# Kernel tuning notes

Hardware: AMD Instinct MI355X
Metric: run time of the kernel (lower is better)

The kernel has to match this reference:

```python
import jax, jax.numpy as jnp
import numpy as np

B, NUM_CLASSES, H, W, CF = 2, 19, 64, 64, 256
TOPK_IDX = 20  # hard-coded in the torch source: sorted descending value at index 20


def _cosine(x):
    # x: [B, N, D] -> clamped cosine affinity [B, N, N]
    xn = x / (jnp.linalg.norm(x, axis=2, keepdims=True) + 1e-9)
    return jnp.maximum(jnp.einsum('bnd,bmd->bnm', xn, xn), 0.0)


def _conv1x1(x, w, b):
    # x: [B, C, H, W], w: [O, C], b: [O]
    return jnp.einsum('bchw,oc->bohw', x, w) + b[None, :, None, None]


def setup_inputs() -> dict:
    key = jax.random.key(0)
    ks = jax.random.split(key, 12)
    s_c = (2.0 / NUM_CLASSES) ** 0.5  # kaiming fan_in scale for 1x1 conv
    s_f = (2.0 / CF) ** 0.5
    return {
        'pred': jax.random.normal(ks[0], (B, NUM_CLASSES, H, W), jnp.float32),
        'feat': jax.random.normal(ks[1], (B, CF, H, W), jnp.float32),
        'w_cls1': jax.random.normal(ks[2], (NUM_CLASSES, NUM_CLASSES), jnp.float32) * s_c,
        'b_cls1': jnp.zeros((NUM_CLASSES,), jnp.float32),
        'w_cls2': jax.random.normal(ks[3], (NUM_CLASSES, NUM_CLASSES), jnp.float32) * s_c,
        'b_cls2': jnp.zeros((NUM_CLASSES,), jnp.float32),
        'w_pro1': jax.random.normal(ks[4], (CF, CF), jnp.float32) * s_f,
        'b_pro1': jnp.zeros((CF,), jnp.float32),
        'w_pro2': jax.random.normal(ks[5], (CF, CF), jnp.float32) * s_f,
        'b_pro2': jnp.zeros((CF,), jnp.float32),
        'class_weight': jnp.ones((NUM_CLASSES,), jnp.float32),
    }


def reference(pred, feat, w_cls1, b_cls1, w_cls2, b_cls2,
              w_pro1, b_pro1, w_pro2, b_pro2, class_weight):
    bsz, c, h, w = feat.shape
    C = pred.shape[1]
    N = h * w
    feat_flat = feat.reshape(bsz, c, N).transpose(0, 2, 1)  # [B, N, 256]

    # --- no_grad block 1: confidence mask + top-k sparsified cosine affinity ---
    prob = jax.nn.softmax(pred, axis=1)
    p_prob = prob.max(axis=1)      # [B, H, W]
    p_max = prob.argmax(axis=1)    # [B, H, W]
    cwm = class_weight / (class_weight.max() + 1e-10) * 0.95
    mask = ((p_prob >= 0.95) | (p_prob >= cwm[p_max])).astype(jnp.float32)
    mask = jax.lax.stop_gradient(mask.reshape(bsz, N, 1))  # broadcast over classes

    aff1 = _cosine(feat_flat)                                # [B, N, N]
    thr = -jnp.sort(-aff1, axis=-1)[:, :, TOPK_IDX:TOPK_IDX + 1]  # per-row 21st largest
    aff1 = jnp.where(aff1 < thr, 0.0, aff1)
    aff1 = jax.lax.stop_gradient(aff1 + aff1.transpose(0, 2, 1))

    # --- degree-normalized propagation of predictions ---
    pred_flat = pred.reshape(bsz, C, N).transpose(0, 2, 1)   # [B, N, C]
    d1 = (aff1.sum(-1) + 1e-10) ** -0.5                      # D^{-1/2}
    aff1n = d1[:, :, None] * aff1 * d1[:, None, :]           # D^{-1/2} A D^{-1/2}
    p2 = jnp.einsum('bnm,bmc->bnc', aff1n, pred_flat)
    p3 = (0.8 * p2 + 0.2 * pred_flat) * (1.0 - mask) + (0.2 * p2 + 0.8 * pred_flat) * mask
    pred2 = p3.transpose(0, 2, 1).reshape(bsz, C, h, w)
    pred_out = _conv1x1(_conv1x1(pred2, w_cls1, b_cls1), w_cls2, b_cls2)

    # --- no_grad block 2: class-consistency-masked affinity over refined softmax ---
    oh = jax.nn.one_hot(p_max, C, dtype=jnp.float32)         # [B, H, W, C]
    # faithful to torch: permute(0,2,3,1) on the already-[B,H,W,C] one-hot, then flat view
    oh = jnp.transpose(oh, (0, 2, 3, 1)).reshape(bsz, -1, C)
    sp = jax.nn.softmax(pred_out, axis=1).reshape(bsz, C, N).transpose(0, 2, 1)
    aff_f = _cosine(sp)
    aff_f = jnp.where(_cosine(oh) == 0.0, 0.0, aff_f)
    d2 = (aff_f.sum(-1) + 1e-10) ** -0.5
    aff_fn = jax.lax.stop_gradient(d2[:, :, None] * aff_f * d2[:, None, :])

    # --- propagate features and project ---
    new_feat = jnp.einsum('bnm,bmc->bnc', aff_fn, feat_flat)
    new_feat = new_feat.transpose(0, 2, 1).reshape(bsz, c, h, w)
    feat_out = _conv1x1(jax.nn.relu(_conv1x1(new_feat, w_pro1, b_pro1)), w_pro2, b_pro2)
    return pred_out, feat_out
```

## Files before the change

kernel.cpp:

```cpp
#include <hip/hip_runtime.h>

#define NN 4096
#define DD 256
#define CC 19
#define BB 2

typedef __attribute__((ext_vector_type(8))) short bf16x8;
typedef _Float16 f16x8 __attribute__((ext_vector_type(8)));
typedef __attribute__((ext_vector_type(4))) float f32x4;

#define GLL16(gp, lp) __builtin_amdgcn_global_load_lds( \
    (const __attribute__((address_space(1))) unsigned int*)(gp), \
    (__attribute__((address_space(3))) unsigned int*)(lp), 16, 0, 0)

__device__ inline unsigned short f2b(float f) {
  unsigned int u = __float_as_uint(f);
  return (unsigned short)((u + 0x7FFFu + ((u >> 16) & 1u)) >> 16);
}
__device__ inline float b2f(unsigned short h) {
  return __uint_as_float(((unsigned int)h) << 16);
}
__device__ inline unsigned int pack2(float a, float b) {
  return (unsigned int)f2b(a) | ((unsigned int)f2b(b) << 16);
}
__device__ inline void split16(float x, unsigned short& h, unsigned short& l) {
  _Float16 hh = (_Float16)x;
  float hf = (float)hh;
  _Float16 ll = (_Float16)((x - hf) * 2048.0f);
  h = *reinterpret_cast<unsigned short*>(&hh);
  l = *reinterpret_cast<unsigned short*>(&ll);
}

__global__ __launch_bounds__(256) void k_prep(const float* __restrict__ pred,
                                              const float* __restrict__ cw,
                                              const float* __restrict__ feat,
                                              float* __restrict__ maskb,
                                              unsigned int* __restrict__ ohbits,
                                              unsigned short* __restrict__ xh,
                                              unsigned short* __restrict__ xl) {
  int g = blockIdx.x * 256 + threadIdx.x;
  int b = g >> 12, n = g & (NN - 1);
  {
    const float* p = pred + (size_t)b * CC * NN + n;
    float v[CC];
    float mx = -1e30f; int am = 0;
#pragma unroll
    for (int c = 0; c < CC; ++c) {
      float t = p[(size_t)c * NN];
      v[c] = t;
      if (t > mx) { mx = t; am = c; }
    }
    float s = 0.f;
#pragma unroll
    for (int c = 0; c < CC; ++c) s += expf(v[c] - mx);
    float pprob = 1.f / s;
    float cmax = 0.f;
#pragma unroll
    for (int c = 0; c < CC; ++c) cmax = fmaxf(cmax, cw[c]);
    float cwm = cw[am] / (cmax + 1e-10f) * 0.95f;
    maskb[g] = (pprob >= 0.95f || pprob >= cwm) ? 1.f : 0.f;
    int h = n >> 6, w = n & 63;
    int L = w * (CC * 64) + am * 64 + h;
    atomicOr(&ohbits[b * NN + L / CC], 1u << (L % CC));
  }
  {
    const float* f = feat + (size_t)b * DD * NN + n;
    float s = 0.f;
    for (int d = 0; d < DD; ++d) { float t = f[(size_t)d * NN]; s += t * t; }
    float r = 1.f / (sqrtf(s) + 1e-9f);
    size_t ob = ((size_t)b * NN + n) * DD;
    for (int d = 0; d < DD; d += 4) {
      ushort4 oh, ol;
      split16(f[(size_t)d * NN] * r, oh.x, ol.x);
      split16(f[(size_t)(d + 1) * NN] * r, oh.y, ol.y);
      split16(f[(size_t)(d + 2) * NN] * r, oh.z, ol.z);
      split16(f[(size_t)(d + 3) * NN] * r, oh.w, ol.w);
      *reinterpret_cast<ushort4*>(&xh[ob + d]) = oh;
      *reinterpret_cast<ushort4*>(&xl[ob + d]) = ol;
    }
  }
}

__global__ __launch_bounds__(256, 2) void k_gram1(const unsigned short* __restrict__ xh,
                                                  const unsigned short* __restrict__ xl,
                                                  float* __restrict__ M) {
  int Lh = blockIdx.x;
  int L = (Lh & 7) * 66 + (Lh >> 3);
  int b = blockIdx.y;
  int I = 0;
  while (L >= 32 - I) { L -= 32 - I; ++I; }
  int J = I + L;
  int i0 = I * 128, j0 = J * 128;
  float* Mb = M + (size_t)b * NN * NN;
  const unsigned short* XH = xh + (size_t)b * NN * DD;
  const unsigned short* XL = xl + (size_t)b * NN * DD;
  __shared__ unsigned short stage[2][4][128][32];
  int t = threadIdx.x;
  int wave = t >> 6, lane = t & 63;
  int wr = (wave & 1) * 64, wc = (wave >> 1) * 64;
  int lrow = lane & 15, quad = lane >> 4;
  int sel = (lrow >> 1) & 3;
  f32x4 accH[4][4] = {}, accL[4][4] = {};
  const unsigned short* src = (wave == 0) ? XH + (size_t)i0 * DD
                             : (wave == 1) ? XL + (size_t)i0 * DD
                             : (wave == 2) ? XH + (size_t)j0 * DD
                                           : XL + (size_t)j0 * DD;
  int srow = lane >> 2;
  int spart = (lane & 3) ^ ((lane >> 3) & 3);
#pragma unroll
  for (int e = 0; e < 8; ++e)
    GLL16(&src[(size_t)(e * 16 + srow) * DD + spart * 8], &stage[0][wave][e * 16][0]);
  __syncthreads();
  int cur = 0;
  for (int k0 = 0; k0 < DD; k0 += 32) {
    if (k0 + 32 < DD) {
#pragma unroll
      for (int e = 0; e < 8; ++e)
        GLL16(&src[(size_t)(e * 16 + srow) * DD + k0 + 32 + spart * 8],
              &stage[cur ^ 1][wave][e * 16][0]);
    }
    f16x8 ah[4], al[4], bh[4], bl[4];
#pragma unroll
    for (int i = 0; i < 4; ++i) {
      int ra = wr + i * 16 + lrow;
      int rb = wc + i * 16 + lrow;
      int sl = (quad ^ sel) * 8;
      ah[i] = *reinterpret_cast<const f16x8*>(&stage[cur][0][ra][sl]);
      al[i] = *reinterpret_cast<const f16x8*>(&stage[cur][1][ra][sl]);
      bh[i] = *reinterpret_cast<const f16x8*>(&stage[cur][2][rb][sl]);
      bl[i] = *reinterpret_cast<const f16x8*>(&stage[cur][3][rb][sl]);
    }
#pragma unroll
    for (int i = 0; i < 4; ++i) {
#pragma unroll
      for (int j = 0; j < 4; ++j) {
        accH[i][j] = __builtin_amdgcn_mfma_f32_16x16x32_f16(ah[i], bh[j], accH[i][j], 0, 0, 0);
        accL[i][j] = __builtin_amdgcn_mfma_f32_16x16x32_f16(ah[i], bl[j], accL[i][j], 0, 0, 0);
        accL[i][j] = __builtin_amdgcn_mfma_f32_16x16x32_f16(al[i], bh[j], accL[i][j], 0, 0, 0);
      }
    }
    __syncthreads();
    cur ^= 1;
  }
#pragma unroll
  for (int i = 0; i < 4; ++i)
#pragma unroll
    for (int j = 0; j < 4; ++j)
#pragma unroll
      for (int reg = 0; reg < 4; ++reg)
        accH[i][j][reg] = fmaxf(accH[i][j][reg] + accL[i][j][reg] * 4.8828125e-4f, 0.f);
  float* buf = (float*)stage;
  int rr = t >> 4, cc = t & 15;
  for (int half = 0; half < 2; ++half) {
    __syncthreads();
    if ((wr >> 6) == half) {
#pragma unroll
      for (int i = 0; i < 4; ++i)
#pragma unroll
        for (int j = 0; j < 4; ++j)
#pragma unroll
          for (int reg = 0; reg < 4; ++reg)
            buf[(i * 16 + quad * 4 + reg) * 132 + wc + j * 16 + lrow] = accH[i][j][reg];
    }
    __syncthreads();
#pragma unroll
    for (int i = 0; i < 4; ++i) {
      int row = rr + i * 16;
#pragma unroll
      for (int q = 0; q < 2; ++q) {
        int col = cc * 4 + q * 64;
        *reinterpret_cast<float4*>(&Mb[(size_t)(i0 + half * 64 + row) * NN + j0 + col]) =
            *reinterpret_cast<float4*>(&buf[row * 132 + col]);
      }
    }
  }
  if (I != J) {
    for (int half = 0; half < 2; ++half) {
      __syncthreads();
      if ((wc >> 6) == half) {
#pragma unroll
        for (int i = 0; i < 4; ++i)
#pragma unroll
          for (int j = 0; j < 4; ++j)
#pragma unroll
            for (int reg = 0; reg < 4; ++reg)
              buf[(j * 16 + lrow) * 132 + wr + i * 16 + quad * 4 + reg] = accH[i][j][reg];
      }
      __syncthreads();
#pragma unroll
      for (int i = 0; i < 4; ++i) {
        int row = rr + i * 16;
#pragma unroll
        for (int q = 0; q < 2; ++q) {
          int col = cc * 4 + q * 64;
          *reinterpret_cast<float4*>(&Mb[(size_t)(j0 + half * 64 + row) * NN + i0 + col]) =
              *reinterpret_cast<float4*>(&buf[row * 132 + col]);
        }
      }
    }
  }
}

__global__ __launch_bounds__(256, 2) void k_topk(const float* __restrict__ M,
                                                 float* __restrict__ thr) {
  __shared__ unsigned int cbuf[4][64];
  int b = blockIdx.y;
  int wave = threadIdx.x >> 6, lane = threadIdx.x & 63;
  int n = blockIdx.x * 4 + wave;
  const float* row = M + (size_t)b * NN * NN + (size_t)n * NN;
  uint4 v[16];
#pragma unroll
  for (int e = 0; e < 16; ++e) {
    unsigned long long addr = (unsigned long long)(row + lane * 4 + e * 256);
    asm volatile("global_load_dwordx4 %0, %1, off" : "=v"(v[e]) : "v"(addr));
  }
  asm volatile("s_waitcnt vmcnt(0)" ::: "memory");
  __builtin_amdgcn_sched_barrier(0);
  unsigned int mx = 0u;
#pragma unroll
  for (int e = 0; e < 16; ++e) {
    unsigned int a = v[e].x > v[e].y ? v[e].x : v[e].y;
    unsigned int c2 = v[e].z > v[e].w ? v[e].z : v[e].w;
    a = a > c2 ? a : c2;
    mx = mx > a ? mx : a;
  }
  unsigned int lo = 0u, hi = 0x3FC00000u;
  while (lo < hi) {
    unsigned int mid = lo + ((hi - lo + 1) >> 1);
    if (__popcll(__ballot(mx >= mid)) >= 21) lo = mid; else hi = mid - 1;
  }
  unsigned int s = lo;
  unsigned int base = 0;
  unsigned long long ltmask = (1ull << lane) - 1ull;
#pragma unroll
  for (int e = 0; e < 16; ++e) {
#pragma unroll
    for (int q = 0; q < 4; ++q) {
      unsigned int val = (q == 0) ? v[e].x : (q == 1) ? v[e].y : (q == 2) ? v[e].z : v[e].w;
      unsigned long long mk = __ballot(val >= s);
      if (mk) {
        unsigned int pos = base + (unsigned int)__popcll(mk & ltmask);
        if (val >= s && pos < 64u) cbuf[wave][pos] = val;
        base += (unsigned int)__popcll(mk);
      }
    }
  }
  asm volatile("s_waitcnt lgkmcnt(0)" ::: "memory");
  __builtin_amdgcn_sched_barrier(0);
  unsigned int t = s;
  if (base <= 64u) {
    unsigned int cand = (lane < (int)base) ? cbuf[wave][lane] : 0u;
    lo = s; hi = 0x3FC00000u;
    while (lo < hi) {
      unsigned int mid = lo + ((hi - lo + 1) >> 1);
      if (__popcll(__ballot(cand >= mid)) >= 21) lo = mid; else hi = mid - 1;
    }
    t = lo;
  }
  {
    unsigned int t1 = t + 1u;
    int c1 = 0, c2 = 0;
#pragma unroll
    for (int e = 0; e < 16; ++e) {
      c1 += (int)__popcll(__ballot(v[e].x >= t));
      c1 += (int)__popcll(__ballot(v[e].y >= t));
      c1 += (int)__popcll(__ballot(v[e].z >= t));
      c1 += (int)__popcll(__ballot(v[e].w >= t));
      c2 += (int)__popcll(__ballot(v[e].x >= t1));
      c2 += (int)__popcll(__ballot(v[e].y >= t1));
      c2 += (int)__popcll(__ballot(v[e].z >= t1));
      c2 += (int)__popcll(__ballot(v[e].w >= t1));
    }
    if (!(c1 >= 21 && c2 < 21)) {
      lo = 0u; hi = 0x40000000u;
      while (lo < hi) {
        unsigned int mid = lo + ((hi - lo + 1) >> 1);
        int c = 0;
#pragma unroll
        for (int e = 0; e < 16; ++e) {
          c += (int)__popcll(__ballot(v[e].x >= mid));
          c += (int)__popcll(__ballot(v[e].y >= mid));
          c += (int)__popcll(__ballot(v[e].z >= mid));
          c += (int)__popcll(__ballot(v[e].w >= mid));
        }
        if (c >= 21) lo = mid; else hi = mid - 1;
      }
      t = lo;
    }
  }
  if (lane == 0) thr[b * NN + n] = __uint_as_float(t);
}

__global__ __launch_bounds__(256) void k_symm(float* __restrict__ M, const float* __restrict__ thr,
                                              float* __restrict__ dsum) {
  int L = blockIdx.x;
  int b = blockIdx.y;
  int I = 0;
  while (L >= 64 - I) { L -= 64 - I; ++I; }
  int J = I + L;
  float* Mb = M + (size_t)b * NN * NN;
  unsigned short* Mus = (unsigned short*)Mb;
  const float* th = thr + b * NN;
  __shared__ float A[64][65];
  int t = threadIdx.x;
  int i0 = I * 64, j0 = J * 64;
  float areg[16];
#pragma unroll
  for (int e = 0; e < 16; ++e) {
    int lin = t + e * 256;
    int i = lin >> 6, j = lin & 63;
    areg[e] = Mb[(size_t)(i0 + i) * NN + j0 + j];
  }
#pragma unroll
  for (int e = 0; e < 16; ++e) {
    int lin = t + e * 256;
    int i = lin >> 6, j = lin & 63;
    float a = areg[e];
    float v = a * ((a >= th[i0 + i] ? 1.f : 0.f) + (a >= th[j0 + j] ? 1.f : 0.f));
    A[i][j] = v;
  }
  __syncthreads();
  {
    int i = t >> 2, seg = (t & 3) * 16;
    float v[16];
#pragma unroll
    for (int q = 0; q < 4; ++q)
      *reinterpret_cast<float4*>(&v[q * 4]) = *reinterpret_cast<float4*>(&A[i][seg + q * 4]);
    unsigned int pk[8];
#pragma unroll
    for (int q = 0; q < 8; ++q) pk[q] = pack2(v[2 * q], v[2 * q + 1]);
    size_t ub = 2 * (size_t)(i0 + i) * NN + 2 * (size_t)j0 + seg;
    *reinterpret_cast<int4*>(&Mus[ub])     = *reinterpret_cast<int4*>(&pk[0]);
    *reinterpret_cast<int4*>(&Mus[ub + 8]) = *reinterpret_cast<int4*>(&pk[4]);
  }
  if (I != J) {
    int j = t >> 2, seg = (t & 3) * 16;
    float v[16];
#pragma unroll
    for (int e = 0; e < 16; ++e) v[e] = A[seg + e][j];
    unsigned int pk[8];
#pragma unroll
    for (int q = 0; q < 8; ++q) pk[q] = pack2(v[2 * q], v[2 * q + 1]);
    size_t ub = 2 * (size_t)(j0 + j) * NN + 2 * (size_t)i0 + seg;
    *reinterpret_cast<int4*>(&Mus[ub])     = *reinterpret_cast<int4*>(&pk[0]);
    *reinterpret_cast<int4*>(&Mus[ub + 8]) = *reinterpret_cast<int4*>(&pk[4]);
  }
  if (t < 64) {
    float s = 0.f;
#pragma unroll
    for (int j = 0; j < 64; ++j) s += A[t][j];
    atomicAdd(&dsum[b * NN + i0 + t], s);
  } else if (t < 128 && I != J) {
    int j = t - 64;
    float s = 0.f;
#pragma unroll
    for (int i = 0; i < 64; ++i) s += A[i][j];
    atomicAdd(&dsum[b * NN + j0 + j], s);
  }
}

__global__ void k_make_yb(const float* __restrict__ pred, const float* __restrict__ d1,
                          unsigned short* __restrict__ ybh) {
  int g = blockIdx.x * 256 + threadIdx.x;
  int idx = g * 4;
  int b = idx / (32 * NN);
  int c = (idx / NN) & 31;
  int n = idx & (NN - 1);
  ushort4 o = make_ushort4(0, 0, 0, 0);
  if (c < CC) {
    float4 p = *reinterpret_cast<const float4*>(&pred[((size_t)b * CC + c) * NN + n]);
    const float* dd = d1 + b * NN + n;
    o.x = f2b(p.x * (1.f / sqrtf(dd[0] + 1e-10f)));
    o.y = f2b(p.y * (1.f / sqrtf(dd[1] + 1e-10f)));
    o.z = f2b(p.z * (1.f / sqrtf(dd[2] + 1e-10f)));
    o.w = f2b(p.w * (1.f / sqrtf(dd[3] + 1e-10f)));
  }
  *reinterpret_cast<ushort4*>(&ybh[idx]) = o;
}

__global__ __launch_bounds__(256, 2) void k_p2_mfma(
    const float* __restrict__ M, const unsigned short* __restrict__ ybh,
    const float* __restrict__ d1, float* __restrict__ p2b) {
  int b = blockIdx.y;
  int n0 = blockIdx.x * 64;
  const unsigned short* Mus = (const unsigned short*)(M + (size_t)b * NN * NN);
  const unsigned short* Y = ybh + (size_t)b * 32 * NN;
  __shared__ unsigned short As2[2][64][64];
  __shared__ unsigned short Ys2[2][32][64];
  int t = threadIdx.x;
  int wave = t >> 6, lane = t & 63;
  int wn = (wave & 1) * 32;
  int wc = (wave >> 1) * 16;
  int lrow = lane & 15, quad = lane >> 4;
  f32x4 acc[2] = {{0.f,0.f,0.f,0.f},{0.f,0.f,0.f,0.f}};
  int lr3 = lane >> 3;
  int srow = wave * 8 + lr3;
  int spart = (lane & 7) ^ lr3;
#pragma unroll
  for (int e = 0; e < 2; ++e)
    GLL16(&Mus[2 * (size_t)(n0 + e * 32 + srow) * NN + spart * 8],
          &As2[0][e * 32 + wave * 8][0]);
  GLL16(&Y[(size_t)srow * NN + spart * 8], &Ys2[0][wave * 8][0]);
  __syncthreads();
  int cur = 0;
  for (int m0 = 0; m0 < NN; m0 += 64) {
    if (m0 + 64 < NN) {
#pragma unroll
      for (int e = 0; e < 2; ++e)
        GLL16(&Mus[2 * (size_t)(n0 + e * 32 + srow) * NN + 2 * (size_t)(m0 + 64) + spart * 8],
              &As2[cur ^ 1][e * 32 + wave * 8][0]);
      GLL16(&Y[(size_t)srow * NN + m0 + 64 + spart * 8], &Ys2[cur ^ 1][wave * 8][0]);
    }
#pragma unroll
    for (int kc = 0; kc < 2; ++kc) {
      int sl = ((kc * 4 + quad) ^ (lrow & 7)) * 8;
      bf16x8 bfr = *reinterpret_cast<const bf16x8*>(&Ys2[cur][wc + lrow][sl]);
#pragma unroll
      for (int i = 0; i < 2; ++i) {
        bf16x8 af = *reinterpret_cast<const bf16x8*>(&As2[cur][wn + i * 16 + lrow][sl]);
        acc[i] = __builtin_amdgcn_mfma_f32_16x16x32_bf16(af, bfr, acc[i], 0, 0, 0);
      }
    }
    __syncthreads();
    cur ^= 1;
  }
  int c = wc + lrow;
  if (c < CC) {
#pragma unroll
    for (int i = 0; i < 2; ++i) {
#pragma unroll
      for (int reg = 0; reg < 4; ++reg) {
        int n = n0 + wn + i * 16 + quad * 4 + reg;
        float dv = 1.f / sqrtf(d1[b * NN + n] + 1e-10f);
        p2b[((size_t)b * NN + n) * CC + c] = dv * acc[i][reg];
      }
    }
  }
}

__global__ __launch_bounds__(64) void k_pred_head(const float* __restrict__ pred,
    const float* __restrict__ p2b, const float* __restrict__ maskb,
    const float* __restrict__ w1, const float* __restrict__ b1,
    const float* __restrict__ w2, const float* __restrict__ b2,
    float* __restrict__ out, unsigned short* __restrict__ spnP) {
  __shared__ float sw1[CC * CC], sw2[CC * CC], sb1[CC], sb2[CC];
  int t = threadIdx.x;
  for (int i = t; i < CC * CC; i += 64) { sw1[i] = w1[i]; sw2[i] = w2[i]; }
  if (t < CC) { sb1[t] = b1[t]; sb2[t] = b2[t]; }
  __syncthreads();
  int g = blockIdx.x * 64 + t;
  int b = g >> 12, n = g & (NN - 1);
  float m = maskb[g];
  float ca = (m > 0.5f) ? 0.2f : 0.8f;
  float cb = (m > 0.5f) ? 0.8f : 0.2f;
  const float* P = pred + (size_t)b * CC * NN + n;
  const float* Q = p2b + (size_t)g * CC;
  float p3[CC];
#pragma unroll
  for (int c = 0; c < CC; ++c) p3[c] = ca * Q[c] + cb * P[(size_t)c * NN];
  float midv[CC];
#pragma unroll
  for (int o = 0; o < CC; ++o) {
    float s = sb1[o];
#pragma unroll
    for (int c = 0; c < CC; ++c) s += sw1[o * CC + c] * p3[c];
    midv[o] = s;
  }
  float ov[CC];
  float mx = -1e30f;
#pragma unroll
  for (int o = 0; o < CC; ++o) {
    float s = sb2[o];
#pragma unroll
    for (int c = 0; c < CC; ++c) s += sw2[o * CC + c] * midv[c];
    ov[o] = s;
    out[(size_t)b * CC * NN + (size_t)o * NN + n] = s;
    mx = fmaxf(mx, s);
  }
  float se = 0.f;
  float e[CC];
#pragma unroll
  for (int o = 0; o < CC; ++o) { e[o] = expf(ov[o] - mx); se += e[o]; }
  float inv = 1.f / se;
  float nrm = 0.f;
#pragma unroll
  for (int o = 0; o < CC; ++o) { float sp = e[o] * inv; e[o] = sp; nrm += sp * sp; }
  float rn = 1.f / (sqrtf(nrm) + 1e-9f);
  unsigned short sp[32];
#pragma unroll
  for (int o = 0; o < CC; ++o) sp[o] = f2b(e[o] * rn);
#pragma unroll
  for (int o = CC; o < 32; ++o) sp[o] = 0;
  unsigned short* dst = spnP + (size_t)g * 32;
#pragma unroll
  for (int q = 0; q < 4; ++q)
    *reinterpret_cast<int4*>(&dst[q * 8]) = *reinterpret_cast<int4*>(&sp[q * 8]);
}

__global__ __launch_bounds__(256) void k_gram2(const unsigned short* __restrict__ spnP,
    const unsigned int* __restrict__ bits, unsigned short* __restrict__ Mh,
    float* __restrict__ d2) {
  int L = blockIdx.x;
  int b = blockIdx.y;
  int I = 0;
  while (L >= 64 - I) { L -= 64 - I; ++I; }
  int J = I + L;
  const unsigned short* X = spnP + (size_t)b * NN * 32;
  unsigned short* Mb = Mh + (size_t)b * NN * NN;
  __shared__ unsigned short As[64][32], Bs[64][32];
  __shared__ unsigned short tr[64][66];
  __shared__ unsigned int bI[64], bJ[64];
  int t = threadIdx.x;
  int wave = t >> 6, lane = t & 63;
  int lrow = lane & 15, quad = lane >> 4;
  int i0 = I * 64, j0 = J * 64;
  int srow = wave * 16 + (lane >> 2);
  int spart = (lane & 3) ^ ((lane >> 3) & 3);
  GLL16(&X[(size_t)(i0 + srow) * 32 + spart * 8], &As[wave * 16][0]);
  GLL16(&X[(size_t)(j0 + srow) * 32 + spart * 8], &Bs[wave * 16][0]);
  if (t < 64) bI[t] = bits[b * NN + i0 + t];
  else if (t < 128) bJ[t - 64] = bits[b * NN + j0 + t - 64];
  __syncthreads();
  int wi = wave & 1, wj = wave >> 1;
  int sl = (quad ^ ((lrow >> 1) & 3)) * 8;
  bf16x8 af[2], bfr[2];
#pragma unroll
  for (int i = 0; i < 2; ++i) {
    af[i]  = *reinterpret_cast<const bf16x8*>(&As[wi * 32 + i * 16 + lrow][sl]);
    bfr[i] = *reinterpret_cast<const bf16x8*>(&Bs[wj * 32 + i * 16 + lrow][sl]);
  }
  f32x4 acc[2][2] = {{{0.f,0.f,0.f,0.f},{0.f,0.f,0.f,0.f}},{{0.f,0.f,0.f,0.f},{0.f,0.f,0.f,0.f}}};
#pragma unroll
  for (int i = 0; i < 2; ++i)
#pragma unroll
    for (int j = 0; j < 2; ++j)
      acc[i][j] = __builtin_amdgcn_mfma_f32_16x16x32_bf16(af[i], bfr[j], acc[i][j], 0, 0, 0);
#pragma unroll
  for (int i = 0; i < 2; ++i) {
#pragma unroll
    for (int j = 0; j < 2; ++j) {
#pragma unroll
      for (int reg = 0; reg < 4; ++reg) {
        int row = wi * 32 + i * 16 + quad * 4 + reg;
        int col = wj * 32 + j * 16 + lrow;
        bool keep = (bI[row] & bJ[col]) != 0u;
        float v = keep ? fmaxf(acc[i][j][reg], 0.f) : 0.f;
        tr[row][col] = f2b(v);
      }
    }
  }
  __syncthreads();
  {
    int row = t >> 2, seg = (t & 3) * 16;
    unsigned int w[8];
#pragma unroll
    for (int k = 0; k < 8; ++k)
      w[k] = *reinterpret_cast<const unsigned int*>(&tr[row][seg + 2 * k]);
    *reinterpret_cast<int4*>(&Mb[(size_t)(i0 + row) * NN + j0 + seg])     =
        *reinterpret_cast<int4*>(&w[0]);
    *reinterpret_cast<int4*>(&Mb[(size_t)(i0 + row) * NN + j0 + seg + 8]) =
        *reinterpret_cast<int4*>(&w[4]);
  }
  if (I != J) {
#pragma unroll
    for (int e = 0; e < 16; ++e) {
      int lin = t + e * 256;
      int jr = lin >> 6, ic = lin & 63;
      Mb[(size_t)(j0 + jr) * NN + i0 + ic] = tr[ic][jr];
    }
  }
  if (t < 64) {
    float s = 0.f;
#pragma unroll
    for (int c = 0; c < 64; ++c) s += b2f(tr[t][c]);
    atomicAdd(&d2[b * NN + i0 + t], s);
  } else if (t < 128 && I != J) {
    int c = t - 64;
    float s = 0.f;
#pragma unroll
    for (int i = 0; i < 64; ++i) s += b2f(tr[i][c]);
    atomicAdd(&d2[b * NN + j0 + c], s);
  }
}

__global__ void k_make_z(const float* __restrict__ feat, const float* __restrict__ d2,
                         unsigned short* __restrict__ zb,
                         const float* __restrict__ w1, const float* __restrict__ w2,
                         unsigned short* __restrict__ wb1, unsigned short* __restrict__ wb2) {
  int g = blockIdx.x * 256 + threadIdx.x;
  int idx = g * 4;
  int b = idx / (DD * NN);
  int m = idx & (NN - 1);
  float4 f = *reinterpret_cast<const float4*>(&feat[idx]);
  const float* dd = d2 + b * NN + m;
  ushort4 o;
  o.x = f2b(f.x * (1.f / sqrtf(dd[0] + 1e-10f)));
  o.y = f2b(f.y * (1.f / sqrtf(dd[1] + 1e-10f)));
  o.z = f2b(f.z * (1.f / sqrtf(dd[2] + 1e-10f)));
  o.w = f2b(f.w * (1.f / sqrtf(dd[3] + 1e-10f)));
  *reinterpret_cast<ushort4*>(&zb[idx]) = o;
  if (blockIdx.x < DD * DD / (4 * 256)) {
    int wi = idx;
    float4 a = *reinterpret_cast<const float4*>(&w1[wi]);
    float4 c = *reinterpret_cast<const float4*>(&w2[wi]);
    ushort4 oa, oc;
    oa.x = f2b(a.x); oa.y = f2b(a.y); oa.z = f2b(a.z); oa.w = f2b(a.w);
    oc.x = f2b(c.x); oc.y = f2b(c.y); oc.z = f2b(c.z); oc.w = f2b(c.w);
    *reinterpret_cast<ushort4*>(&wb1[wi]) = oa;
    *reinterpret_cast<ushort4*>(&wb2[wi]) = oc;
  }
}

__global__ __launch_bounds__(256, 2) void k_newfeat_mfma(
    const unsigned short* __restrict__ Mh, const unsigned short* __restrict__ zb,
    const float* __restrict__ d2, unsigned short* __restrict__ nfh) {
  int b = blockIdx.z;
  int nblk = blockIdx.x;
  int dblk = blockIdx.y;
  const unsigned short* A = zb + (size_t)b * DD * NN + (size_t)(dblk * 64) * NN;
  const unsigned short* Bm = Mh + (size_t)b * NN * NN + (size_t)(nblk * 64) * NN;
  __shared__ unsigned short As[2][64][64];
  __shared__ unsigned short Bs[2][64][64];
  int t = threadIdx.x;
  int wave = t >> 6, lane = t & 63;
  int wd = (wave & 1) * 32, wn = (wave >> 1) * 32;
  int lrow = lane & 15, quad = lane >> 4;
  f32x4 acc[2][2] = {{{0.f,0.f,0.f,0.f},{0.f,0.f,0.f,0.f}},{{0.f,0.f,0.f,0.f},{0.f,0.f,0.f,0.f}}};
  int lr3 = lane >> 3;
  int srow = wave * 8 + lr3;
  int spart = (lane & 7) ^ lr3;
#pragma unroll
  for (int e = 0; e < 2; ++e) {
    GLL16(&A [(size_t)(e * 32 + srow) * NN + spart * 8], &As[0][e * 32 + wave * 8][0]);
    GLL16(&Bm[(size_t)(e * 32 + srow) * NN + spart * 8], &Bs[0][e * 32 + wave * 8][0]);
  }
  __syncthreads();
  int cur = 0;
  for (int m0 = 0; m0 < NN; m0 += 64) {
    if (m0 + 64 < NN) {
#pragma unroll
      for (int e = 0; e < 2; ++e) {
        GLL16(&A [(size_t)(e * 32 + srow) * NN + m0 + 64 + spart * 8],
              &As[cur ^ 1][e * 32 + wave * 8][0]);
        GLL16(&Bm[(size_t)(e * 32 + srow) * NN + m0 + 64 + spart * 8],
              &Bs[cur ^ 1][e * 32 + wave * 8][0]);
      }
    }
#pragma unroll
    for (int kc = 0; kc < 2; ++kc) {
      int sl = ((kc * 4 + quad) ^ (lrow & 7)) * 8;
      bf16x8 af[2], bfr[2];
#pragma unroll
      for (int i = 0; i < 2; ++i) {
        af[i]  = *reinterpret_cast<const bf16x8*>(&As[cur][wd + i * 16 + lrow][sl]);
        bfr[i] = *reinterpret_cast<const bf16x8*>(&Bs[cur][wn + i * 16 + lrow][sl]);
      }
#pragma unroll
      for (int i = 0; i < 2; ++i)
#pragma unroll
        for (int j = 0; j < 2; ++j)
          acc[i][j] = __builtin_amdgcn_mfma_f32_16x16x32_bf16(af[i], bfr[j], acc[i][j], 0, 0, 0);
    }
    __syncthreads();
    cur ^= 1;
  }
#pragma unroll
  for (int j = 0; j < 2; ++j) {
    int n = nblk * 64 + wn + j * 16 + lrow;
    float sc = 1.f / sqrtf(d2[b * NN + n] + 1e-10f);
#pragma unroll
    for (int i = 0; i < 2; ++i) {
      int d = dblk * 64 + wd + i * 16 + quad * 4;
      ushort4 o;
      o.x = f2b(acc[i][j].x * sc); o.y = f2b(acc[i][j].y * sc);
      o.z = f2b(acc[i][j].z * sc); o.w = f2b(acc[i][j].w * sc);
      *reinterpret_cast<ushort4*>(&nfh[((size_t)b * NN + n) * DD + d]) = o;
    }
  }
}

__global__ __launch_bounds__(256) void k_conv1_mfma(
    const unsigned short* __restrict__ nfh, const unsigned short* __restrict__ wb1,
    const float* __restrict__ b1, unsigned short* __restrict__ midh) {
  int b = blockIdx.z;
  int nblk = blockIdx.x;
  int oblk = blockIdx.y;
  int n0 = nblk * 64, o0 = oblk * 64;
  __shared__ unsigned short As[64][72];
  __shared__ unsigned short Bs[64][72];
  int t = threadIdx.x;
  int wave = t >> 6, lane = t & 63;
  int wn = (wave & 1) * 32, wo = (wave >> 1) * 32;
  int lrow = lane & 15, quad = lane >> 4;
  f32x4 acc[2][2] = {{{0.f,0.f,0.f,0.f},{0.f,0.f,0.f,0.f}},{{0.f,0.f,0.f,0.f},{0.f,0.f,0.f,0.f}}};
  int sr = t >> 3, sc = (t & 7) * 8;
  for (int d0 = 0; d0 < DD; d0 += 64) {
#pragma unroll
    for (int e = 0; e < 2; ++e) {
      int rr = sr + e * 32;
      *reinterpret_cast<int4*>(&As[rr][sc]) =
          *reinterpret_cast<const int4*>(&nfh[((size_t)b * NN + n0 + rr) * DD + d0 + sc]);
      *reinterpret_cast<int4*>(&Bs[rr][sc]) =
          *reinterpret_cast<const int4*>(&wb1[(size_t)(o0 + rr) * DD + d0 + sc]);
    }
    __syncthreads();
#pragma unroll
    for (int kc = 0; kc < 2; ++kc) {
      int ko = kc * 32 + quad * 8;
      bf16x8 af[2], bfr[2];
#pragma unroll
      for (int i = 0; i < 2; ++i) {
        af[i]  = *reinterpret_cast<const bf16x8*>(&As[wn + i * 16 + lrow][ko]);
        bfr[i] = *reinterpret_cast<const bf16x8*>(&Bs[wo + i * 16 + lrow][ko]);
      }
#pragma unroll
      for (int i = 0; i < 2; ++i)
#pragma unroll
        for (int j = 0; j < 2; ++j)
          acc[i][j] = __builtin_amdgcn_mfma_f32_16x16x32_bf16(af[i], bfr[j], acc[i][j], 0, 0, 0);
    }
    __syncthreads();
  }
#pragma unroll
  for (int j = 0; j < 2; ++j) {
    int o = o0 + wo + j * 16 + lrow;
    float bias = b1[o];
#pragma unroll
    for (int i = 0; i < 2; ++i) {
      int nb = n0 + wn + i * 16 + quad * 4;
      ushort4 v;
      v.x = f2b(fmaxf(acc[i][j].x + bias, 0.f));
      v.y = f2b(fmaxf(acc[i][j].y + bias, 0.f));
      v.z = f2b(fmaxf(acc[i][j].z + bias, 0.f));
      v.w = f2b(fmaxf(acc[i][j].w + bias, 0.f));
      *reinterpret_cast<ushort4*>(&midh[((size_t)b * DD + o) * NN + nb]) = v;
    }
  }
}

__global__ __launch_bounds__(256) void k_conv2_mfma(
    const unsigned short* __restrict__ midh, const unsigned short* __restrict__ wb2,
    const float* __restrict__ b2, float* __restrict__ outp) {
  int b = blockIdx.z;
  int nblk = blockIdx.x;
  int oblk = blockIdx.y;
  int n0 = nblk * 64, o0 = oblk * 64;
  __shared__ unsigned short As[64][72];
  __shared__ unsigned short Bs[64][72];
  int t = threadIdx.x;
  int wave = t >> 6, lane = t & 63;
  int wn = (wave & 1) * 32, wo = (wave >> 1) * 32;
  int lrow = lane & 15, quad = lane >> 4;
  f32x4 acc[2][2] = {{{0.f,0.f,0.f,0.f},{0.f,0.f,0.f,0.f}},{{0.f,0.f,0.f,0.f},{0.f,0.f,0.f,0.f}}};
  int sr = t >> 3, sc = (t & 7) * 8;
  for (int d0 = 0; d0 < DD; d0 += 64) {
#pragma unroll
    for (int e = 0; e < 2; ++e) {
      int rr = sr + e * 32;
      *reinterpret_cast<int4*>(&Bs[rr][sc]) =
          *reinterpret_cast<const int4*>(&wb2[(size_t)(o0 + rr) * DD + d0 + sc]);
      unsigned short v[8];
      *reinterpret_cast<int4*>(v) =
          *reinterpret_cast<const int4*>(&midh[((size_t)b * DD + d0 + rr) * NN + n0 + sc]);
#pragma unroll
      for (int j = 0; j < 8; ++j) As[sc + j][rr] = v[j];
    }
    __syncthreads();
#pragma unroll
    for (int kc = 0; kc < 2; ++kc) {
      int ko = kc * 32 + quad * 8;
      bf16x8 af[2], bfr[2];
#pragma unroll
      for (int i = 0; i < 2; ++i) {
        af[i]  = *reinterpret_cast<const bf16x8*>(&As[wn + i * 16 + lrow][ko]);
        bfr[i] = *reinterpret_cast<const bf16x8*>(&Bs[wo + i * 16 + lrow][ko]);
      }
#pragma unroll
      for (int i = 0; i < 2; ++i)
#pragma unroll
        for (int j = 0; j < 2; ++j)
          acc[i][j] = __builtin_amdgcn_mfma_f32_16x16x32_bf16(af[i], bfr[j], acc[i][j], 0, 0, 0);
    }
    __syncthreads();
  }
#pragma unroll
  for (int j = 0; j < 2; ++j) {
    int o = o0 + wo + j * 16 + lrow;
    float bias = b2[o];
#pragma unroll
    for (int i = 0; i < 2; ++i) {
      int nb = n0 + wn + i * 16 + quad * 4;
      float4 v = make_float4(acc[i][j].x + bias, acc[i][j].y + bias,
                             acc[i][j].z + bias, acc[i][j].w + bias);
      *reinterpret_cast<float4*>(&outp[((size_t)b * DD + o) * NN + nb]) = v;
    }
  }
}

extern "C" void kernel_launch(void* const* d_in, const int* in_sizes, int n_in,
                              void* d_out, int out_size, void* d_ws, size_t ws_size,
                              hipStream_t stream) {
  (void)in_sizes; (void)n_in; (void)out_size; (void)ws_size;
  const float* pred   = (const float*)d_in[0];
  const float* feat   = (const float*)d_in[1];
  const float* w_cls1 = (const float*)d_in[2];
  const float* b_cls1 = (const float*)d_in[3];
  const float* w_cls2 = (const float*)d_in[4];
  const float* b_cls2 = (const float*)d_in[5];
  const float* w_pro1 = (const float*)d_in[6];
  const float* b_pro1 = (const float*)d_in[7];
  const float* w_pro2 = (const float*)d_in[8];
  const float* b_pro2 = (const float*)d_in[9];
  const float* cw     = (const float*)d_in[10];
  float* out = (float*)d_out;

  float* Mbuf = (float*)d_ws;
  float* spnT = Mbuf + (size_t)BB * NN * NN;
  float* p2b  = spnT + (size_t)BB * CC * NN;
  float* thr  = p2b + (size_t)BB * NN * CC;
  float* dsum = thr + BB * NN;
  float* d2s  = dsum + BB * NN;
  unsigned int* ohbits = (unsigned int*)(d2s + BB * NN);
  float* maskb = (float*)(ohbits + BB * NN);
  unsigned short* xh   = (unsigned short*)(maskb + BB * NN);
  unsigned short* xl   = xh + (size_t)BB * NN * DD;
  unsigned short* nfh  = xl + (size_t)BB * NN * DD;
  unsigned short* midh = nfh + (size_t)BB * NN * DD;
  unsigned short* zb   = midh + (size_t)BB * DD * NN;
  unsigned short* wb1  = zb + (size_t)BB * DD * NN;
  unsigned short* wb2  = wb1 + (size_t)DD * DD;
  unsigned short* ybh  = wb2 + (size_t)DD * DD;
  unsigned short* Mh   = (unsigned short*)Mbuf;
  unsigned short* spnP = (unsigned short*)spnT;

  hipMemsetAsync(dsum, 0, sizeof(float) * 3 * BB * NN, stream);

  k_prep<<<BB * NN / 256, 256, 0, stream>>>(pred, cw, feat, maskb, ohbits, xh, xl);
  k_gram1<<<dim3(528, BB), 256, 0, stream>>>(xh, xl, Mbuf);
  k_topk<<<dim3(NN / 4, BB), 256, 0, stream>>>(Mbuf, thr);
  k_symm<<<dim3(2080, BB), 256, 0, stream>>>(Mbuf, thr, dsum);
  k_make_yb<<<BB * 32 * NN / 4 / 256, 256, 0, stream>>>(pred, dsum, ybh);
  k_p2_mfma<<<dim3(NN / 64, BB), 256, 0, stream>>>(Mbuf, ybh, dsum, p2b);
  k_pred_head<<<BB * NN / 64, 64, 0, stream>>>(pred, p2b, maskb, w_cls1, b_cls1,
                                               w_cls2, b_cls2, out, spnP);
  k_gram2<<<dim3(2080, BB), 256, 0, stream>>>(spnP, ohbits, Mh, d2s);
  k_make_z<<<BB * DD * NN / 4 / 256, 256, 0, stream>>>(feat, d2s, zb,
                                                       w_pro1, w_pro2, wb1, wb2);
  k_newfeat_mfma<<<dim3(64, 4, BB), 256, 0, stream>>>(Mh, zb, d2s, nfh);
  k_conv1_mfma<<<dim3(64, 4, BB), 256, 0, stream>>>(nfh, wb1, b_pro1, midh);
  k_conv2_mfma<<<dim3(64, 4, BB), 256, 0, stream>>>(midh, wb2, b_pro2,
                                                    out + (size_t)BB * CC * NN);
}
```

Baseline: 331.2 us.

## Retile symmetric gram kernel to 128x64 tiles with doubled grid

```diff
diff --git a/kernel.cpp b/kernel.cpp
--- a/kernel.cpp
+++ b/kernel.cpp
@@ -81,69 +81,80 @@
   }
 }
 
-__global__ __launch_bounds__(256, 2) void k_gram1(const unsigned short* __restrict__ xh,
-                                                  const unsigned short* __restrict__ xl,
-                                                  float* __restrict__ M) {
+__global__ __launch_bounds__(256) void k_gram1(const unsigned short* __restrict__ xh,
+                                               const unsigned short* __restrict__ xl,
+                                               float* __restrict__ M) {
   int Lh = blockIdx.x;
-  int L = (Lh & 7) * 66 + (Lh >> 3);
+  int L = (Lh & 7) * 132 + (Lh >> 3);
   int b = blockIdx.y;
   int I = 0;
-  while (L >= 32 - I) { L -= 32 - I; ++I; }
-  int J = I + L;
-  int i0 = I * 128, j0 = J * 128;
+  while (L >= 64 - 2 * I) { L -= 64 - 2 * I; ++I; }
+  int J = 2 * I + L;
+  int i0 = I * 128, j0 = J * 64;
+  bool mirror = (J >= 2 * I + 2);
   float* Mb = M + (size_t)b * NN * NN;
   const unsigned short* XH = xh + (size_t)b * NN * DD;
   const unsigned short* XL = xl + (size_t)b * NN * DD;
-  __shared__ unsigned short stage[2][4][128][32];
+  __shared__ unsigned short stage[2][384][32];
   int t = threadIdx.x;
   int wave = t >> 6, lane = t & 63;
-  int wr = (wave & 1) * 64, wc = (wave >> 1) * 64;
+  int wr = wave * 32;
   int lrow = lane & 15, quad = lane >> 4;
   int sel = (lrow >> 1) & 3;
-  f32x4 accH[4][4] = {}, accL[4][4] = {};
-  const unsigned short* src = (wave == 0) ? XH + (size_t)i0 * DD
-                             : (wave == 1) ? XL + (size_t)i0 * DD
-                             : (wave == 2) ? XH + (size_t)j0 * DD
-                                           : XL + (size_t)j0 * DD;
+  f32x4 accH[2][4] = {}, accL[2][4] = {};
   int srow = lane >> 2;
   int spart = (lane & 3) ^ ((lane >> 3) & 3);
 #pragma unroll
-  for (int e = 0; e < 8; ++e)
-    GLL16(&src[(size_t)(e * 16 + srow) * DD + spart * 8], &stage[0][wave][e * 16][0]);
+  for (int e = 0; e < 6; ++e) {
+    int k = wave * 6 + e;
+    const unsigned short* pl; int r0;
+    if (k < 8)       { pl = XH; r0 = i0 + k * 16; }
+    else if (k < 16) { pl = XL; r0 = i0 + (k - 8) * 16; }
+    else if (k < 20) { pl = XH; r0 = j0 + (k - 16) * 16; }
+    else             { pl = XL; r0 = j0 + (k - 20) * 16; }
+    GLL16(&pl[(size_t)(r0 + srow) * DD + spart * 8], &stage[0][k * 16][0]);
+  }
   __syncthreads();
   int cur = 0;
   for (int k0 = 0; k0 < DD; k0 += 32) {
     if (k0 + 32 < DD) {
 #pragma unroll
-      for (int e = 0; e < 8; ++e)
-        GLL16(&src[(size_t)(e * 16 + srow) * DD + k0 + 32 + spart * 8],
-              &stage[cur ^ 1][wave][e * 16][0]);
-    }
-    f16x8 ah[4], al[4], bh[4], bl[4];
-#pragma unroll
-    for (int i = 0; i < 4; ++i) {
+      for (int e = 0; e < 6; ++e) {
+        int k = wave * 6 + e;
+        const unsigned short* pl; int r0;
+        if (k < 8)       { pl = XH; r0 = i0 + k * 16; }
+        else if (k < 16) { pl = XL; r0 = i0 + (k - 8) * 16; }
+        else if (k < 20) { pl = XH; r0 = j0 + (k - 16) * 16; }
+        else             { pl = XL; r0 = j0 + (k - 20) * 16; }
+        GLL16(&pl[(size_t)(r0 + srow) * DD + k0 + 32 + spart * 8],
+              &stage[cur ^ 1][k * 16][0]);
+      }
+    }
+    int sl = (quad ^ sel) * 8;
+    f16x8 ah[2], al[2];
+#pragma unroll
+    for (int i = 0; i < 2; ++i) {
       int ra = wr + i * 16 + lrow;
-      int rb = wc + i * 16 + lrow;
-      int sl = (quad ^ sel) * 8;
-      ah[i] = *reinterpret_cast<const f16x8*>(&stage[cur][0][ra][sl]);
-      al[i] = *reinterpret_cast<const f16x8*>(&stage[cur][1][ra][sl]);
-      bh[i] = *reinterpret_cast<const f16x8*>(&stage[cur][2][rb][sl]);
-      bl[i] = *reinterpret_cast<const f16x8*>(&stage[cur][3][rb][sl]);
-    }
-#pragma unroll
-    for (int i = 0; i < 4; ++i) {
-#pragma unroll
-      for (int j = 0; j < 4; ++j) {
-        accH[i][j] = __builtin_amdgcn_mfma_f32_16x16x32_f16(ah[i], bh[j], accH[i][j], 0, 0, 0);
-        accL[i][j] = __builtin_amdgcn_mfma_f32_16x16x32_f16(ah[i], bl[j], accL[i][j], 0, 0, 0);
-        accL[i][j] = __builtin_amdgcn_mfma_f32_16x16x32_f16(al[i], bh[j], accL[i][j], 0, 0, 0);
+      ah[i] = *reinterpret_cast<const f16x8*>(&stage[cur][ra][sl]);
+      al[i] = *reinterpret_cast<const f16x8*>(&stage[cur][128 + ra][sl]);
+    }
+#pragma unroll
+    for (int j = 0; j < 4; ++j) {
+      int rb = j * 16 + lrow;
+      f16x8 bh = *reinterpret_cast<const f16x8*>(&stage[cur][256 + rb][sl]);
+      f16x8 bl = *reinterpret_cast<const f16x8*>(&stage[cur][320 + rb][sl]);
+#pragma unroll
+      for (int i = 0; i < 2; ++i) {
+        accH[i][j] = __builtin_amdgcn_mfma_f32_16x16x32_f16(ah[i], bh, accH[i][j], 0, 0, 0);
+        accL[i][j] = __builtin_amdgcn_mfma_f32_16x16x32_f16(ah[i], bl, accL[i][j], 0, 0, 0);
+        accL[i][j] = __builtin_amdgcn_mfma_f32_16x16x32_f16(al[i], bh, accL[i][j], 0, 0, 0);
       }
     }
     __syncthreads();
     cur ^= 1;
   }
 #pragma unroll
-  for (int i = 0; i < 4; ++i)
+  for (int i = 0; i < 2; ++i)
 #pragma unroll
     for (int j = 0; j < 4; ++j)
 #pragma unroll
@@ -155,47 +166,39 @@
     __syncthreads();
     if ((wr >> 6) == half) {
 #pragma unroll
-      for (int i = 0; i < 4; ++i)
+      for (int i = 0; i < 2; ++i)
 #pragma unroll
         for (int j = 0; j < 4; ++j)
 #pragma unroll
           for (int reg = 0; reg < 4; ++reg)
-            buf[(i * 16 + quad * 4 + reg) * 132 + wc + j * 16 + lrow] = accH[i][j][reg];
+            buf[((wr & 63) + i * 16 + quad * 4 + reg) * 132 + j * 16 + lrow] = accH[i][j][reg];
     }
     __syncthreads();
 #pragma unroll
     for (int i = 0; i < 4; ++i) {
       int row = rr + i * 16;
-#pragma unroll
-      for (int q = 0; q < 2; ++q) {
-        int col = cc * 4 + q * 64;
-        *reinterpret_cast<float4*>(&Mb[(size_t)(i0 + half * 64 + row) * NN + j0 + col]) =
-            *reinterpret_cast<float4*>(&buf[row * 132 + col]);
-      }
-    }
-  }
-  if (I != J) {
+      *reinterpret_cast<float4*>(&Mb[(size_t)(i0 + half * 64 + row) * NN + j0 + cc * 4]) =
+          *reinterpret_cast<float4*>(&buf[row * 132 + cc * 4]);
+    }
+  }
+  if (mirror) {
     for (int half = 0; half < 2; ++half) {
       __syncthreads();
-      if ((wc >> 6) == half) {
-#pragma unroll
-        for (int i = 0; i < 4; ++i)
+      if ((wr >> 6) == half) {
+#pragma unroll
+        for (int i = 0; i < 2; ++i)
 #pragma unroll
           for (int j = 0; j < 4; ++j)
 #pragma unroll
             for (int reg = 0; reg < 4; ++reg)
-              buf[(j * 16 + lrow) * 132 + wr + i * 16 + quad * 4 + reg] = accH[i][j][reg];
+              buf[(j * 16 + lrow) * 132 + (wr & 63) + i * 16 + quad * 4 + reg] = accH[i][j][reg];
       }
       __syncthreads();
 #pragma unroll
       for (int i = 0; i < 4; ++i) {
         int row = rr + i * 16;
-#pragma unroll
-        for (int q = 0; q < 2; ++q) {
-          int col = cc * 4 + q * 64;
-          *reinterpret_cast<float4*>(&Mb[(size_t)(j0 + half * 64 + row) * NN + i0 + col]) =
-              *reinterpret_cast<float4*>(&buf[row * 132 + col]);
-        }
+        *reinterpret_cast<float4*>(&Mb[(size_t)(j0 + row) * NN + i0 + half * 64 + cc * 4]) =
+            *reinterpret_cast<float4*>(&buf[row * 132 + cc * 4]);
       }
     }
   }
@@ -836,7 +839,7 @@
   hipMemsetAsync(dsum, 0, sizeof(float) * 3 * BB * NN, stream);
 
   k_prep<<<BB * NN / 256, 256, 0, stream>>>(pred, cw, feat, maskb, ohbits, xh, xl);
-  k_gram1<<<dim3(528, BB), 256, 0, stream>>>(xh, xl, Mbuf);
+  k_gram1<<<dim3(1056, BB), 256, 0, stream>>>(xh, xl, Mbuf);
   k_topk<<<dim3(NN / 4, BB), 256, 0, stream>>>(Mbuf, thr);
   k_symm<<<dim3(2080, BB), 256, 0, stream>>>(Mbuf, thr, dsum);
   k_make_yb<<<BB * 32 * NN / 4 / 256, 256, 0, stream>>>(pred, dsum, ybh);
```

Result: no change. 337.6 us (+1.9%).
